# Optimization experiments

Hardware: AMD Instinct MI355X
Metric: run time of the kernel (lower is better)

## Reference

```python
import jax, jax.numpy as jnp
import numpy as np

CUTOFF, WIDTH, DIM, N_CONV = 5.0, 0.1, 64, 3
N_CENTERS = int(np.ceil(CUTOFF / WIDTH))            # 50
CENTERS = np.linspace(0.0, CUTOFF, N_CENTERS)       # RBF centers
GAP = float(CENTERS[1] - CENTERS[0])                # center spacing, coef = -1/GAP


def sp(x):
    # torch.nn.Softplus(beta=0.5, threshold=14): linear when 0.5*x > 14
    return jnp.where(x > 28.0, x, 2.0 * jax.nn.softplus(0.5 * x))


def setup_inputs() -> dict:
    key = jax.random.key(0)
    ks = jax.random.split(key, 32)
    N, E, K, NSEL, ESEL = 50000, 1600000, 20000, 5000, 20000
    f = jnp.float32
    nrm = lambda k, s, sc=0.1: jax.random.normal(k, s, dtype=f) * sc
    inp = {
        "emb": nrm(ks[0], (100, DIM), 1.0),
        "dist": jax.random.uniform(ks[1], (E,), f, 0.1, CUTOFF),
        "edge_mask": nrm(ks[2], (N_CENTERS,)),
        "conv_w1": nrm(ks[3], (N_CONV, DIM, DIM)),
        "cf_w1": nrm(ks[4], (N_CONV, DIM, N_CENTERS)),
        "cf_b1": nrm(ks[5], (N_CONV, DIM)),
        "cf_w2": nrm(ks[6], (N_CONV, DIM, DIM)),
        "cf_b2": nrm(ks[7], (N_CONV, DIM)),
        "nl2_w": nrm(ks[8], (N_CONV, DIM, DIM)),
        "nl2_b": nrm(ks[9], (N_CONV, DIM)),
        "nl3_w": nrm(ks[10], (N_CONV, DIM, DIM)),
        "nl3_b": nrm(ks[11], (N_CONV, DIM)),
        "nt1_w": nrm(ks[12], (32, DIM)),
        "nt1_b": nrm(ks[13], (32,)),
        "nt2_w": nrm(ks[14], (3, 32)),
        "nt2_b": nrm(ks[15], (3,)),
        "et1_w": nrm(ks[16], (64, 2 * DIM)),
        "et1_b": nrm(ks[17], (64,)),
        "et2_w": nrm(ks[18], (5, 64)),
        "et2_b": nrm(ks[19], (5,)),
        "node_type": jax.random.randint(ks[20], (N,), 0, 100),
        "src": jax.random.randint(ks[21], (E,), 0, N),
        "dst": jax.random.randint(ks[22], (E,), 0, N),
        "select_edge_index": jax.random.randint(ks[23], (K,), 0, E),
        "node_index": jax.random.randint(ks[24], (NSEL,), 0, N),
        "source_index": jax.random.randint(ks[25], (ESEL,), 0, N),
        "target_index": jax.random.randint(ks[26], (ESEL,), 0, N),
    }
    return inp


def reference(emb, dist, edge_mask, conv_w1, cf_w1, cf_b1, cf_w2, cf_b2,
              nl2_w, nl2_b, nl3_w, nl3_b, nt1_w, nt1_b, nt2_w, nt2_b,
              et1_w, et1_b, et2_w, et2_b,
              node_type, src, dst, select_edge_index, node_index,
              source_index, target_index):
    N = node_type.shape[0]
    centers = jnp.asarray(CENTERS, dtype=dist.dtype)
    # RBF edge features [E, 50]: exp(-(d - c)^2 / gap)
    rbf = jnp.exp((-1.0 / GAP) * (dist[:, None] - centers[None, :]) ** 2)
    # overwrite masked edges with learned edge_mask vector
    rbf = rbf.at[select_edge_index].set(edge_mask.astype(rbf.dtype))
    node = emb[node_type]                               # [N, 64]
    for i in range(N_CONV):                             # Interaction layers
        new_node = node @ conv_w1[i].T                  # bias-free projection
        h = sp(rbf @ cf_w1[i].T + cf_b1[i]) @ cf_w2[i].T + cf_b2[i]   # [E,64] filters
        msg = new_node[src] * h                         # u_mul_e
        agg = jax.ops.segment_sum(msg, dst, num_segments=N)          # sum reduce
        node = node + (sp(agg @ nl2_w[i].T + nl2_b[i]) @ nl3_w[i].T + nl3_b[i])
    ns = node[node_index]                               # [NSEL, 64]
    node_logits = (ns @ nt1_w.T + nt1_b) @ nt2_w.T + nt2_b           # [NSEL, 3]
    ef = jnp.concatenate([node[source_index], node[target_index]], axis=1)  # [ESEL,128]
    edge_logits = (ef @ et1_w.T + et1_b) @ et2_w.T + et2_b           # [ESEL, 5]
    return node_logits, edge_logits
```

## Files before the change

kernel.cpp:

```cpp
#include <hip/hip_runtime.h>
#include <hip/hip_bf16.h>

#define DIM 64
#define NC 50
#define TABN 4096
#define TABP (TABN + 2)
#define EPB 2048
#define NBMAX 512

typedef short bf16x8 __attribute__((ext_vector_type(8)));
typedef float f32x4  __attribute__((ext_vector_type(4)));
#define MFMA(a,b,c) __builtin_amdgcn_mfma_f32_16x16x32_bf16(a,b,c,0,0,0)

__device__ __forceinline__ float sp_f(float x){
  float e = __expf(0.5f*x);
  float s = 2.0f*__logf(1.0f+e);
  return x > 28.0f ? x : s;
}

__device__ __forceinline__ float rdl(float v, int l){
  return __int_as_float(__builtin_amdgcn_readlane(__float_as_int(v), l));
}

__device__ __forceinline__ unsigned short b16(float x){
  __hip_bfloat16 h = __float2bfloat16(x);
  return __builtin_bit_cast(unsigned short, h);
}

__device__ __forceinline__ void wsplit(float x, unsigned short& h, unsigned short& l){
  h = b16(x);
  float hf = __uint_as_float(((unsigned int)h) << 16);
  l = b16(x - hf);
}


__global__ __launch_bounds__(256) void bhist_kernel(const int* __restrict__ dst,
                                                    unsigned int* __restrict__ gbcnt,
                                                    unsigned int* __restrict__ flagbits,
                                                    int E, int NB, int FW){
  __shared__ unsigned int cnt[NBMAX];
  int tid = threadIdx.x;
  for (int b=tid; b<NB; b+=256) cnt[b] = 0;
  __syncthreads();
  int e0 = blockIdx.x*EPB, eend = min(e0+EPB, E);
  for (int e=e0+tid; e<eend; e+=256) atomicAdd(&cnt[dst[e]>>7], 1u);
  for (int w = blockIdx.x*256+tid; w < FW; w += gridDim.x*256) flagbits[w] = 0;
  __syncthreads();
  for (int b=tid; b<NB; b+=256) if (cnt[b]) atomicAdd(&gbcnt[b], cnt[b]);
}

__global__ void sel_mark_kernel(const int* __restrict__ sel,
                                unsigned int* __restrict__ flagbits, int K){
  int id = blockIdx.x*256 + threadIdx.x;
  if (id < K){ int e = sel[id]; atomicOr(&flagbits[e>>5], 1u << (e&31)); }
}

__global__ __launch_bounds__(NBMAX) void bscan_kernel(const unsigned int* __restrict__ gbcnt,
                                                      unsigned int* __restrict__ bscan,
                                                      unsigned int* __restrict__ gcursor,
                                                      int* __restrict__ offs,
                                                      int NB, int N, int E){
  __shared__ unsigned int s[NBMAX];
  int tid = threadIdx.x;
  unsigned int v = (tid < NB) ? gbcnt[tid] : 0;
  s[tid] = v;
  __syncthreads();
  for (int off=1; off<NBMAX; off<<=1){
    unsigned int u = (tid >= off) ? s[tid-off] : 0;
    __syncthreads();
    s[tid] += u;
    __syncthreads();
  }
  unsigned int excl = s[tid] - v;
  if (tid < NB){ bscan[tid] = excl; gcursor[tid] = excl; }
  if (tid == NB-1) bscan[NB] = excl + v;
  if (tid == 0) offs[N] = E;
}

__global__ __launch_bounds__(256) void passA_kernel(const int* __restrict__ dst,
                                                    const int* __restrict__ src,
                                                    const float* __restrict__ dist,
                                                    const unsigned int* __restrict__ flagbits,
                                                    unsigned int* __restrict__ gcursor,
                                                    unsigned long long* __restrict__ bbuf,
                                                    int E, int NB){
  __shared__ unsigned int cnt[NBMAX];
  __shared__ unsigned int base[NBMAX];
  int tid = threadIdx.x;
  for (int b=tid; b<NB; b+=256) cnt[b] = 0;
  __syncthreads();
  int e0 = blockIdx.x*EPB, eend = min(e0+EPB, E);
  for (int e=e0+tid; e<eend; e+=256) atomicAdd(&cnt[dst[e]>>7], 1u);
  __syncthreads();
  for (int b=tid; b<NB; b+=256){
    unsigned int c = cnt[b];
    base[b] = c ? atomicAdd(&gcursor[b], c) : 0u;
    cnt[b] = 0;
  }
  __syncthreads();
  for (int e=e0+tid; e<eend; e+=256){
    int d = dst[e];
    int b = d >> 7;
    unsigned int loc = atomicAdd(&cnt[b], 1u);
    float t = fminf(dist[e], 5.f) * ((float)TABN/5.0f);
    int idx = (int)(t + 0.5f); if (idx > TABN) idx = TABN;
    if ((flagbits[e>>5] >> (e&31)) & 1u) idx = TABN+1;
    unsigned int lo = ((unsigned int)src[e] << 16) | (unsigned int)idx;
    unsigned int hi = (unsigned int)(d & 127);
    bbuf[base[b] + loc] = ((unsigned long long)hi << 32) | lo;
  }
}

__global__ __launch_bounds__(256) void passB_kernel(const unsigned long long* __restrict__ bbuf,
                                                    const unsigned int* __restrict__ bscan,
                                                    int* __restrict__ offs,
                                                    unsigned int* __restrict__ csr,
                                                    int N){
  __shared__ unsigned int cnt[128];
  __shared__ unsigned int excl[128];
  int b = blockIdx.x, tid = threadIdx.x;
  unsigned int s0 = bscan[b];
  int m = (int)(bscan[b+1] - s0);
  if (tid < 128) cnt[tid] = 0;
  __syncthreads();
  for (int i=tid; i<m; i+=256)
    atomicAdd(&cnt[(unsigned int)(bbuf[s0+i] >> 32)], 1u);
  __syncthreads();
  if (tid < 128) excl[tid] = cnt[tid];
  __syncthreads();
  for (int off=1; off<128; off<<=1){
    unsigned int v = (tid < 128 && tid >= off) ? excl[tid-off] : 0;
    __syncthreads();
    if (tid < 128) excl[tid] += v;
    __syncthreads();
  }
  int node0 = b << 7;
  if (tid < 128){
    unsigned int ex = excl[tid] - cnt[tid];
    int n = node0 + tid;
    if (n < N) offs[n] = (int)(s0 + ex);
    excl[tid] = ex;
    cnt[tid] = 0;
  }
  __syncthreads();
  for (int i=tid; i<m; i+=256){
    unsigned long long v = bbuf[s0+i];
    unsigned int hi = (unsigned int)(v >> 32);
    unsigned int loc = atomicAdd(&cnt[hi], 1u);
    csr[s0 + excl[hi] + loc] = (unsigned int)v;
  }
}


__global__ void prep_transpose_kernel(const float* __restrict__ cf_w2,
                                      const float* __restrict__ et1_w,
                                      const float* __restrict__ nt1_w,
                                      const float* __restrict__ cf_w1,
                                      float* __restrict__ w2t,
                                      float* __restrict__ et1t,
                                      float* __restrict__ nt1t,
                                      float* __restrict__ w1t){
  int id = blockIdx.x*256 + threadIdx.x;
  if (id < 3*4096){
    int i = id >> 12, r = id & 4095;
    int k = r >> 6, j = r & 63;
    w2t[id]  = cf_w2[i*4096 + j*64 + k];
  }
  if (id < 128*64){
    int k = id >> 6, j = id & 63;
    et1t[id] = et1_w[j*128 + k];
  }
  if (id < 64*32){
    int k = id >> 5, j = id & 31;
    nt1t[id] = nt1_w[j*64 + k];
  }
  if (id < 3*NC*DIM){
    int l = id / (NC*DIM);
    int r = id - l*(NC*DIM);
    int m = r >> 6, k = r & 63;
    w1t[id] = cf_w1[l*DIM*NC + k*NC + m];
  }
}


__global__ void wprep2_kernel(const float* __restrict__ cw1,
                              const float* __restrict__ nl2,
                              const float* __restrict__ nl3,
                              bf16x8* __restrict__ wfrag){
  int id = blockIdx.x*256 + threadIdx.x;
  if (id >= 9*8*64) return;
  int lane = id & 63;
  int f8 = (id >> 6) & 7;
  int m  = id >> 9;
  int nt = f8 >> 1, ks = f8 & 1;
  const float* W = (m < 3) ? (cw1 + m*4096)
                 : (m < 6) ? (nl2 + (m-3)*4096)
                           : (nl3 + (m-6)*4096);
  int j  = nt*16 + (lane & 15);
  int k0 = ks*32 + (lane >> 4)*8;
  bf16x8 vh, vl;
  #pragma unroll
  for (int u=0;u<8;u++){
    unsigned short h,l;
    wsplit(W[j*64 + k0 + u], h, l);
    vh[u] = (short)h; vl[u] = (short)l;
  }
  int fb = m*16 + nt*4 + ks*2;
  wfrag[(fb+0)*64 + lane] = vh;
  wfrag[(fb+1)*64 + lane] = vl;
}


__global__ __launch_bounds__(256) void table_kernel(const float* __restrict__ edge_mask,
                                                    const float* __restrict__ w1t,
                                                    const float* __restrict__ cf_b1,
                                                    const float* __restrict__ w2t,
                                                    const float* __restrict__ cf_b2,
                                                    __hip_bfloat16* __restrict__ tabb){
  int row = blockIdx.x*4 + (threadIdx.x >> 6);
  if (row >= 3*TABP) return;
  int l = row / TABP, p = row - l*TABP;
  int lane = threadIdx.x & 63;
  float rbfv = 0.f;
  if (lane < NC){
    if (p == TABN+1) rbfv = edge_mask[lane];
    else {
      float d = (float)p * (5.0f/(float)TABN);
      float c = (lane == NC-1) ? 5.0f : (float)((double)lane * (5.0/49.0));
      float df = d - c;
      rbfv = __expf((float)(-1.0/(5.0/49.0)) * df * df);
    }
  }
  const float* W1 = w1t + l*NC*DIM;
  float t = cf_b1[l*DIM + lane];
  #pragma unroll 10
  for (int m=0;m<NC;m++)
    t = fmaf(rdl(rbfv, m), W1[m*64 + lane], t);
  float su = sp_f(t);
  const float* W2 = w2t + l*DIM*DIM;
  float h = cf_b2[l*DIM + lane];
  #pragma unroll 16
  for (int k=0;k<DIM;k++)
    h = fmaf(rdl(su, k), W2[k*64 + lane], h);
  tabb[((size_t)l*TABP + p)*DIM + lane] = __float2bfloat16(h);
}


__device__ __forceinline__ bf16x8 ldfrag(const char* base, int rowbase, int ks, int lane){
  int r = lane & 15;
  int off = (ks<<6) + ((lane>>4)<<4);
  return *(const bf16x8*)(base + (rowbase + r)*128 + (off ^ ((r & 7)<<4)));
}

__device__ __forceinline__ void stx(char* XH, char* XLo, int row, int col, float v){
  unsigned short h,l;
  wsplit(v, h, l);
  int off = row*128 + ((col*2) ^ ((row&7)<<4));
  *(unsigned short*)(XH + off) = h;
  *(unsigned short*)(XLo + off) = l;
}

#define MM6G(WF, NT, ACC) \
  { ACC = MFMA(ah0, (WF)[((NT)*4+0)*64 + lane], ACC); \
    ACC = MFMA(ah1, (WF)[((NT)*4+2)*64 + lane], ACC); \
    ACC = MFMA(ah0, (WF)[((NT)*4+1)*64 + lane], ACC); \
    ACC = MFMA(ah1, (WF)[((NT)*4+3)*64 + lane], ACC); \
    ACC = MFMA(al0, (WF)[((NT)*4+0)*64 + lane], ACC); \
    ACC = MFMA(al1, (WF)[((NT)*4+2)*64 + lane], ACC); }

#define LDA(XH_, XLo_) \
  bf16x8 ah0 = ldfrag(XH_, mb, 0, lane), ah1 = ldfrag(XH_, mb, 1, lane); \
  bf16x8 al0 = ldfrag(XLo_, mb, 0, lane), al1 = ldfrag(XLo_, mb, 1, lane);

__global__ __launch_bounds__(256) void node_init8_kernel(const float* __restrict__ emb,
                                                         const int* __restrict__ node_type,
                                                         const bf16x8* __restrict__ wf0,
                                                         float* __restrict__ node,
                                                         unsigned short* __restrict__ nout, int N){
  __shared__ __align__(16) char XP[16384];
  char *XH = XP, *XLo = XP + 8192;
  int tid = threadIdx.x, lane = tid & 63, wv = tid >> 6;
  int nb = blockIdx.x*64, mb = wv*16;
  #pragma unroll
  for (int t=0;t<16;t++){
    int row = mb + t, n = nb + row;
    int ty = (n < N) ? node_type[n] : 0;
    float v = emb[(long)ty*64 + lane];
    if (n < N) node[(long)n*64 + lane] = v;
    stx(XH, XLo, row, lane, v);
  }
  __syncthreads();
  LDA(XH, XLo)
  #pragma unroll
  for (int nt=0; nt<4; nt++){
    f32x4 acc = {0.f,0.f,0.f,0.f};
    MM6G(wf0, nt, acc)
    int col = nt*16 + (lane&15);
    #pragma unroll
    for (int v=0; v<4; v++){
      int n = nb + mb + ((lane>>4)<<2) + v;
      if (n < N) nout[(long)n*64 + col] = b16(acc[v]);
    }
  }
}

template<bool PRODUCE_NN>
__global__ __launch_bounds__(256) void node_update8_kernel(float* __restrict__ node,
                                                           const float* __restrict__ agg,
                                                           const bf16x8* __restrict__ wfA,
                                                           const float* __restrict__ nl2_b,
                                                           const bf16x8* __restrict__ wfB,
                                                           const float* __restrict__ nl3_b,
                                                           const bf16x8* __restrict__ wfC,
                                                           unsigned short* __restrict__ nout, int N){
  __shared__ __align__(16) char XP[16384];
  char *XH = XP, *XLo = XP + 8192;
  int tid = threadIdx.x, lane = tid & 63, wv = tid >> 6;
  int nb = blockIdx.x*64, mb = wv*16;
  #pragma unroll
  for (int t=0;t<16;t++){
    int row = mb + t, n = nb + row;
    float v = (n < N) ? agg[(long)n*64 + lane] : 0.f;
    stx(XH, XLo, row, lane, v);
  }
  __syncthreads();
  {
    LDA(XH, XLo)
    #pragma unroll
    for (int nt=0; nt<4; nt++){
      float bb = nl2_b[nt*16 + (lane&15)];
      f32x4 acc = {bb,bb,bb,bb};
      MM6G(wfA, nt, acc)
      int col = nt*16 + (lane&15);
      #pragma unroll
      for (int v=0; v<4; v++){
        int row = mb + ((lane>>4)<<2) + v;
        stx(XH, XLo, row, col, sp_f(acc[v]));
      }
    }
  }
  {
    LDA(XH, XLo)
    #pragma unroll
    for (int nt=0; nt<4; nt++){
      float bb = nl3_b[nt*16 + (lane&15)];
      f32x4 acc = {bb,bb,bb,bb};
      MM6G(wfB, nt, acc)
      int col = nt*16 + (lane&15);
      #pragma unroll
      for (int v=0; v<4; v++){
        int row = mb + ((lane>>4)<<2) + v;
        int n = nb + row;
        float nv = 0.f;
        if (n < N){
          long g = (long)n*64 + col;
          nv = node[g] + acc[v];
          node[g] = nv;
        }
        stx(XH, XLo, row, col, nv);
      }
    }
  }
  if (PRODUCE_NN){
    LDA(XH, XLo)
    #pragma unroll
    for (int nt=0; nt<4; nt++){
      f32x4 acc = {0.f,0.f,0.f,0.f};
      MM6G(wfC, nt, acc)
      int col = nt*16 + (lane&15);
      #pragma unroll
      for (int v=0; v<4; v++){
        int n = nb + mb + ((lane>>4)<<2) + v;
        if (n < N) nout[(long)n*64 + col] = b16(acc[v]);
      }
    }
  }
}

__global__ __launch_bounds__(256) void agg_kernel(const unsigned int* __restrict__ csr,
                                                  const int* __restrict__ offs,
                                                  const unsigned short* __restrict__ tab,
                                                  const unsigned short* __restrict__ nnb,
                                                  float* __restrict__ agg, int N){
  int n = blockIdx.x*4 + (threadIdx.x >> 6);
  int lane = threadIdx.x & 63;
  if (n >= N) return;
  int beg = offs[n], end = offs[n+1];
  float acc = 0.f;
  for (int c = beg; c < end; c += 64){
    int m = end - c; if (m > 64) m = 64;
    unsigned int pkv = csr[c + (lane < m ? lane : 0)];
    int q = 0;
    for (; q + 8 <= m; q += 8){
      #pragma unroll
      for (int u=0; u<8; u++){
        unsigned int p = (unsigned int)__builtin_amdgcn_readlane((int)pkv, q+u);
        int idx = p & 0xFFFF, s = p >> 16;
        float a  = __uint_as_float(((unsigned int)tab[idx*64 + lane]) << 16);
        float nn = __uint_as_float(((unsigned int)nnb[(long)s*64 + lane]) << 16);
        acc = fmaf(nn, a, acc);
      }
    }
    for (; q < m; q++){
      unsigned int p = (unsigned int)__builtin_amdgcn_readlane((int)pkv, q);
      int idx = p & 0xFFFF, s = p >> 16;
      float a  = __uint_as_float(((unsigned int)tab[idx*64 + lane]) << 16);
      float nn = __uint_as_float(((unsigned int)nnb[(long)s*64 + lane]) << 16);
      acc = fmaf(nn, a, acc);
    }
  }
  agg[(long)n*64 + lane] = acc;
}


__global__ __launch_bounds__(256) void node_head_kernel(const float* __restrict__ node,
                                                        const int* __restrict__ nidx,
                                                        const float* __restrict__ nt1t,
                                                        const float* __restrict__ nt1_b,
                                                        const float* __restrict__ nt2_w,
                                                        const float* __restrict__ nt2_b,
                                                        float* __restrict__ out, int NSEL){
  int r = __builtin_amdgcn_readfirstlane(blockIdx.x*4 + (threadIdx.x>>6));
  int lane = threadIdx.x & 63;
  if (r >= NSEL) return;
  long n = nidx[r];
  const float* x = node + n*64;
  float u = 0.f;
  if (lane < 32){
    u = nt1_b[lane];
    #pragma unroll
    for (int k=0;k<DIM;k++) u += x[k]*nt1t[k*32 + lane];
  }
  #pragma unroll
  for (int q=0;q<3;q++){
    float v = (lane < 32) ? u*nt2_w[q*32 + lane] : 0.f;
    #pragma unroll
    for (int o=32;o>=1;o>>=1) v += __shfl_xor(v, o);
    if (lane == 0) out[(long)r*3 + q] = nt2_b[q] + v;
  }
}

__global__ __launch_bounds__(256) void edge_head_kernel(const float* __restrict__ node,
                                                        const int* __restrict__ sidx,
                                                        const int* __restrict__ tidx,
                                                        const float* __restrict__ et1t,
                                                        const float* __restrict__ et1_b,
                                                        const float* __restrict__ et2_w,
                                                        const float* __restrict__ et2_b,
                                                        float* __restrict__ out, int ESEL){
  int wid = threadIdx.x >> 6, lane = threadIdx.x & 63;
  int r0 = (blockIdx.x*4 + wid)*4;
  if (r0 >= ESEL) return;
  float xs[4], xt[4], acc[4];
  #pragma unroll
  for (int i=0;i<4;i++){
    int r = r0+i < ESEL ? r0+i : ESEL-1;
    long s = sidx[r], t = tidx[r];
    xs[i] = node[s*64 + lane];
    xt[i] = node[t*64 + lane];
    acc[i] = et1_b[lane];
  }
  #pragma unroll 16
  for (int k=0;k<DIM;k++){
    float w1 = et1t[k*64 + lane];
    float w2 = et1t[(64+k)*64 + lane];
    #pragma unroll
    for (int i=0;i<4;i++){
      acc[i] = fmaf(rdl(xs[i], k), w1, acc[i]);
      acc[i] = fmaf(rdl(xt[i], k), w2, acc[i]);
    }
  }
  #pragma unroll
  for (int i=0;i<4;i++){
    if (r0+i >= ESEL) break;
    #pragma unroll
    for (int q=0;q<5;q++){
      float v = acc[i]*et2_w[q*64 + lane];
      #pragma unroll
      for (int o=32;o>=1;o>>=1) v += __shfl_xor(v, o);
      if (lane == 0) out[(long)(r0+i)*5 + q] = et2_b[q] + v;
    }
  }
}


extern "C" void kernel_launch(void* const* d_in, const int* in_sizes, int n_in,
                              void* d_out, int out_size, void* d_ws, size_t ws_size,
                              hipStream_t stream){
  const float* emb      = (const float*)d_in[0];
  const float* dist     = (const float*)d_in[1];
  const float* edge_mask= (const float*)d_in[2];
  const float* conv_w1  = (const float*)d_in[3];
  const float* cf_w1    = (const float*)d_in[4];
  const float* cf_b1    = (const float*)d_in[5];
  const float* cf_w2    = (const float*)d_in[6];
  const float* cf_b2    = (const float*)d_in[7];
  const float* nl2_w    = (const float*)d_in[8];
  const float* nl2_b    = (const float*)d_in[9];
  const float* nl3_w    = (const float*)d_in[10];
  const float* nl3_b    = (const float*)d_in[11];
  const float* nt1_w    = (const float*)d_in[12];
  const float* nt1_b    = (const float*)d_in[13];
  const float* nt2_w    = (const float*)d_in[14];
  const float* nt2_b    = (const float*)d_in[15];
  const float* et1_w    = (const float*)d_in[16];
  const float* et1_b    = (const float*)d_in[17];
  const float* et2_w    = (const float*)d_in[18];
  const float* et2_b    = (const float*)d_in[19];
  const int* node_type  = (const int*)d_in[20];
  const int* src        = (const int*)d_in[21];
  const int* dst        = (const int*)d_in[22];
  const int* sel        = (const int*)d_in[23];
  const int* node_index = (const int*)d_in[24];
  const int* source_index = (const int*)d_in[25];
  const int* target_index = (const int*)d_in[26];

  int E    = in_sizes[1];
  int N    = in_sizes[20];
  int K    = in_sizes[23];
  int NSEL = in_sizes[24];
  int ESEL = in_sizes[25];

  int NB  = (N + 127) >> 7;
  int FW  = (E + 31) >> 5;
  int nbE = (E + EPB - 1) / EPB;

  size_t N64 = (size_t)N*64;
  unsigned long long* bbuf = (unsigned long long*)d_ws;
  float* agg = (float*)d_ws;
  size_t aggsz = ((size_t)2*E > N64) ? (size_t)2*E : N64;
  float* p = (float*)d_ws + aggsz;
  float* node     = p; p += N64;
  unsigned short* nnb = (unsigned short*)p; p += N64/2;
  float* w2t      = p; p += 3*4096;
  float* et1t     = p; p += 128*64;
  float* nt1t     = p; p += 64*32;
  float* w1t      = p; p += 3*NC*DIM;
  bf16x8* wfrag   = (bf16x8*)p; p += 9*16*64*4;
  __hip_bfloat16* tabb = (__hip_bfloat16*)p; p += (size_t)3*TABP*DIM/2;
  unsigned int* csr      = (unsigned int*)p; p += E;
  unsigned int* flagbits = (unsigned int*)p; p += FW;
  unsigned int* gbcnt    = (unsigned int*)p; p += NB;
  unsigned int* bscan    = (unsigned int*)p; p += NB+1;
  unsigned int* gcursor  = (unsigned int*)p; p += NB;
  int* offs              = (int*)p; p += N+1;

  hipMemsetAsync(gbcnt, 0, (size_t)NB*sizeof(int), stream);
  bhist_kernel<<<nbE, 256, 0, stream>>>(dst, gbcnt, flagbits, E, NB, FW);
  sel_mark_kernel<<<(K+255)/256, 256, 0, stream>>>(sel, flagbits, K);
  prep_transpose_kernel<<<48, 256, 0, stream>>>(cf_w2, et1_w, nt1_w, cf_w1,
                                                w2t, et1t, nt1t, w1t);
  wprep2_kernel<<<18, 256, 0, stream>>>(conv_w1, nl2_w, nl3_w, wfrag);
  bscan_kernel<<<1, NBMAX, 0, stream>>>(gbcnt, bscan, gcursor, offs, NB, N, E);
  passA_kernel<<<nbE, 256, 0, stream>>>(dst, src, dist, flagbits, gcursor, bbuf, E, NB);
  passB_kernel<<<NB, 256, 0, stream>>>(bbuf, bscan, offs, csr, N);
  table_kernel<<<(3*TABP+3)/4, 256, 0, stream>>>(edge_mask, w1t, cf_b1, w2t, cf_b2, tabb);

  int nbP  = (N+63)/64;
  int nb_agg = (N+3)/4;
  node_init8_kernel<<<nbP, 256, 0, stream>>>(emb, node_type, wfrag, node, nnb, N);
  for (int l=0;l<3;l++){
    agg_kernel<<<nb_agg, 256, 0, stream>>>(csr, offs,
        (const unsigned short*)(tabb + (size_t)l*TABP*DIM), nnb, agg, N);
    if (l < 2)
      node_update8_kernel<true><<<nbP, 256, 0, stream>>>(node, agg,
          wfrag + (3+l)*16*64, nl2_b + l*64,
          wfrag + (6+l)*16*64, nl3_b + l*64,
          wfrag + (1+l)*16*64, nnb, N);
    else
      node_update8_kernel<false><<<nbP, 256, 0, stream>>>(node, agg,
          wfrag + (3+l)*16*64, nl2_b + l*64,
          wfrag + (6+l)*16*64, nl3_b + l*64,
          nullptr, nullptr, N);
  }

  node_head_kernel<<<(NSEL+3)/4, 256, 0, stream>>>(node, node_index,
      nt1t, nt1_b, nt2_w, nt2_b, (float*)d_out, NSEL);
  edge_head_kernel<<<(ESEL+15)/16, 256, 0, stream>>>(node, source_index, target_index,
      et1t, et1_b, et2_w, et2_b, (float*)d_out + (size_t)NSEL*3, ESEL);
}
```

Measured before the change: 329.3 us.

## Stage bucketed edges in LDS for coalesced scatter in passA

```diff
diff --git a/kernel.cpp b/kernel.cpp
--- a/kernel.cpp
+++ b/kernel.cpp
@@ -5,7 +5,7 @@
 #define NC 50
 #define TABN 4096
 #define TABP (TABN + 2)
-#define EPB 2048
+#define EPB 4096
 #define NBMAX 512
 
 typedef short bf16x8 __attribute__((ext_vector_type(8)));
@@ -85,29 +85,65 @@
                                                     unsigned long long* __restrict__ bbuf,
                                                     int E, int NB){
   __shared__ unsigned int cnt[NBMAX];
-  __shared__ unsigned int base[NBMAX];
-  int tid = threadIdx.x;
+  __shared__ unsigned int gdst[NBMAX];
+  __shared__ unsigned int wpart[4];
+  __shared__ unsigned long long lbuf[EPB];
+  int tid = threadIdx.x, lane = tid & 63, wv = tid >> 6;
   for (int b=tid; b<NB; b+=256) cnt[b] = 0;
   __syncthreads();
-  int e0 = blockIdx.x*EPB, eend = min(e0+EPB, E);
-  for (int e=e0+tid; e<eend; e+=256) atomicAdd(&cnt[dst[e]>>7], 1u);
-  __syncthreads();
-  for (int b=tid; b<NB; b+=256){
-    unsigned int c = cnt[b];
-    base[b] = c ? atomicAdd(&gcursor[b], c) : 0u;
-    cnt[b] = 0;
-  }
-  __syncthreads();
-  for (int e=e0+tid; e<eend; e+=256){
-    int d = dst[e];
-    int b = d >> 7;
-    unsigned int loc = atomicAdd(&cnt[b], 1u);
-    float t = fminf(dist[e], 5.f) * ((float)TABN/5.0f);
-    int idx = (int)(t + 0.5f); if (idx > TABN) idx = TABN;
+  int e0 = blockIdx.x*EPB;
+  int m = E - e0; if (m > EPB) m = EPB;
+  int dreg[16];
+  #pragma unroll
+  for (int i=0;i<16;i++){
+    int li = tid + 256*i;
+    dreg[i] = (li < m) ? dst[e0 + li] : -1;
+    if (dreg[i] >= 0) atomicAdd(&cnt[dreg[i]>>7], 1u);
+  }
+  __syncthreads();
+  int t2 = tid*2;
+  unsigned c0 = (t2 < NB) ? cnt[t2] : 0;
+  unsigned c1 = (t2+1 < NB) ? cnt[t2+1] : 0;
+  unsigned pv = c0 + c1, x = pv;
+  #pragma unroll
+  for (int off=1; off<64; off<<=1){ unsigned u = __shfl_up(x, off); if (lane >= off) x += u; }
+  if (lane == 63) wpart[wv] = x;
+  __syncthreads();
+  unsigned wb = 0;
+  #pragma unroll
+  for (int q=0;q<4;q++) wb += (q < wv) ? wpart[q] : 0;
+  unsigned ex0 = wb + x - pv;
+  unsigned ex1 = ex0 + c0;
+  if (t2 < NB){
+    unsigned gb = c0 ? atomicAdd(&gcursor[t2], c0) : 0u;
+    gdst[t2] = gb - ex0;
+    cnt[t2]  = ex0;
+  }
+  if (t2+1 < NB){
+    unsigned gb = c1 ? atomicAdd(&gcursor[t2+1], c1) : 0u;
+    gdst[t2+1] = gb - ex1;
+    cnt[t2+1]  = ex1;
+  }
+  __syncthreads();
+  #pragma unroll
+  for (int i=0;i<16;i++){
+    if (dreg[i] < 0) continue;
+    int li = tid + 256*i;
+    int e = e0 + li;
+    int d = dreg[i];
+    unsigned pos = atomicAdd(&cnt[d>>7], 1u);
+    float tq = fminf(dist[e], 5.f) * ((float)TABN/5.0f);
+    int idx = (int)(tq + 0.5f); if (idx > TABN) idx = TABN;
     if ((flagbits[e>>5] >> (e&31)) & 1u) idx = TABN+1;
-    unsigned int lo = ((unsigned int)src[e] << 16) | (unsigned int)idx;
-    unsigned int hi = (unsigned int)(d & 127);
-    bbuf[base[b] + loc] = ((unsigned long long)hi << 32) | lo;
+    unsigned lo = ((unsigned int)src[e] << 16) | (unsigned int)idx;
+    lbuf[pos] = ((unsigned long long)(unsigned int)d << 32) | lo;
+  }
+  __syncthreads();
+  for (int i=tid; i<m; i+=256){
+    unsigned long long v = lbuf[i];
+    unsigned d = (unsigned int)(v >> 32);
+    unsigned addr = gdst[d>>7] + (unsigned int)i;
+    bbuf[addr] = (v & 0xFFFFFFFFull) | ((unsigned long long)(d & 127u) << 32);
   }
 }
 
```

Result: faster. 307.7 us (-6.6%).
